# Kernel optimization log

Hardware: AMD Instinct MI355X
Metric: run time of the kernel (lower is better)

The kernel has to match this reference:

```python
import jax, jax.numpy as jnp
import numpy as np

N_WIRES = 4
DIM = 2 ** N_WIRES  # 16-dim statevector


def _zsigns():
    # PauliZ sign per basis state; wire 0 is the most-significant bit
    idx = np.arange(DIM)
    signs = np.stack([1 - 2 * ((idx >> (N_WIRES - 1 - w)) & 1) for w in range(N_WIRES)], 0)
    return jnp.asarray(signs, jnp.float32)  # [4, 16]

ZSIGNS = _zsigns()


def _apply_rx(state, ang, w):
    # state: [B, 16] complex64, ang: [B] rotation angle on wire w
    B = state.shape[0]
    s = state.reshape(B, 2 ** w, 2, 2 ** (N_WIRES - 1 - w))
    c = jnp.cos(ang * 0.5)[:, None, None]
    sn = jnp.sin(ang * 0.5)[:, None, None]
    s0, s1 = s[:, :, 0, :], s[:, :, 1, :]
    o0 = c * s0 - 1j * sn * s1
    o1 = -1j * sn * s0 + c * s1
    return jnp.stack([o0, o1], axis=2).reshape(B, DIM)


def _cnot(state, c, t):
    # flip target bit t where control bit c == 1
    B = state.shape[0]
    s = state.reshape((B,) + (2,) * N_WIRES)
    ca, ta = c + 1, t + 1  # +1 for batch axis
    s0 = jnp.take(s, 0, axis=ca)
    s1 = jnp.take(s, 1, axis=ca)
    t_ax = ta - 1 if ta > ca else ta  # target axis shifts after control axis removed
    s1 = jnp.flip(s1, axis=t_ax)     # size-2 flip == Pauli-X
    return jnp.stack([s0, s1], axis=ca).reshape(B, DIM)


def _qgate(v, theta):
    # v: [B, 4] encoder angles, theta: [4] trainable RX angles (RX angles add)
    B = v.shape[0]
    ang = v + theta[None, :]
    state = jnp.zeros((B, DIM), jnp.complex64).at[:, 0].set(1.0)
    for w in range(N_WIRES):
        state = _apply_rx(state, ang[:, w], w)
    for w in range(N_WIRES):
        state = _cnot(state, w, (w + 1) % N_WIRES)
    probs = jnp.real(state * jnp.conj(state))  # [B, 16]
    return probs @ ZSIGNS.T                    # [B, 4] <Z> per wire


def setup_inputs() -> dict:
    key = jax.random.key(0)
    ks = jax.random.split(key, 16)
    B, S, V, E, H, T = 256, 128, 32000, 256, 4, 32
    d_in = E + H
    sc = 1.0 / np.sqrt(d_in)
    inp = {
        'x': jax.random.randint(ks[0], (B, S), 0, V),
        'embedding': jax.random.normal(ks[1], (V, E), jnp.float32) * 0.02,
        'Wf': jax.random.normal(ks[2], (H, d_in), jnp.float32) * sc,
        'bf': jnp.zeros((H,), jnp.float32),
        'Wi': jax.random.normal(ks[3], (H, d_in), jnp.float32) * sc,
        'bi': jnp.zeros((H,), jnp.float32),
        'Wu': jax.random.normal(ks[4], (H, d_in), jnp.float32) * sc,
        'bu': jnp.zeros((H,), jnp.float32),
        'Wo': jax.random.normal(ks[5], (H, d_in), jnp.float32) * sc,
        'bo': jnp.zeros((H,), jnp.float32),
        'theta_f': jax.random.uniform(ks[6], (H,), jnp.float32, 0.0, 2 * np.pi),
        'theta_i': jax.random.uniform(ks[7], (H,), jnp.float32, 0.0, 2 * np.pi),
        'theta_u': jax.random.uniform(ks[8], (H,), jnp.float32, 0.0, 2 * np.pi),
        'theta_o': jax.random.uniform(ks[9], (H,), jnp.float32, 0.0, 2 * np.pi),
        'Wc': jax.random.normal(ks[10], (T, H), jnp.float32) * 0.5,
        'bc': jnp.zeros((T,), jnp.float32),
    }
    return inp


def reference(x, embedding, Wf, bf, Wi, bi, Wu, bu, Wo, bo,
              theta_f, theta_i, theta_u, theta_o, Wc, bc):
    emb = embedding[x]  # [B, S, E]
    B, S, E = emb.shape
    H = Wf.shape[0]

    def step(carry, xt):
        hx, cx = carry
        comb = jnp.concatenate([xt, hx], axis=1)  # [B, E+H]
        f = jax.nn.sigmoid(_qgate(comb @ Wf.T + bf, theta_f))
        i = jax.nn.sigmoid(_qgate(comb @ Wi.T + bi, theta_i))
        g = jnp.tanh(_qgate(comb @ Wu.T + bu, theta_u))
        o = jax.nn.sigmoid(_qgate(comb @ Wo.T + bo, theta_o))
        cx = f * cx + i * g
        hx = o * jnp.tanh(cx)
        return (hx, cx), hx

    h0 = jnp.zeros((B, H), emb.dtype)
    (_, _), hs = jax.lax.scan(step, (h0, h0), jnp.swapaxes(emb, 0, 1))
    lstm_out = jnp.swapaxes(hs, 0, 1)        # [B, S, H]
    logits = lstm_out @ Wc.T + bc            # [B, S, T]
    return jax.nn.log_softmax(logits, axis=-1)
```

## Files before the change

kernel.cpp:

```cpp
#include <hip/hip_runtime.h>
#include <math.h>

constexpr int NB = 256;
constexpr int NS = 128;
constexpr int NE = 256;
constexpr int DIN = 260;

typedef float f2 __attribute__((ext_vector_type(2)));
#define fma2(A, B, C) __builtin_elementwise_fma((A), (B), (C))

constexpr float INV2PI = 0.15915494309189535f;

__device__ __forceinline__ float rcp_fast(float x) {
#if __has_builtin(__builtin_amdgcn_rcpf)
    return __builtin_amdgcn_rcpf(x);
#else
    return 1.0f / x;
#endif
}

__device__ __forceinline__ float cos_rev(float x) {
    float f, r;
    asm("v_fract_f32 %0, %1" : "=v"(f) : "v"(x));
    asm("v_cos_f32 %0, %1" : "=v"(r) : "v"(f));
    return r;
}

#if __has_builtin(__builtin_amdgcn_mov_dpp)
#define DPP_XOR1(x) __int_as_float(__builtin_amdgcn_mov_dpp(__float_as_int(x), 0xB1, 0xF, 0xF, true))
#define DPP_XOR2(x) __int_as_float(__builtin_amdgcn_mov_dpp(__float_as_int(x), 0x4E, 0xF, 0xF, true))
#define DPP_XOR3(x) __int_as_float(__builtin_amdgcn_mov_dpp(__float_as_int(x), 0x1B, 0xF, 0xF, true))
#else
#define DPP_XOR1(x) __shfl_xor((x), 1, 64)
#define DPP_XOR2(x) __shfl_xor((x), 2, 64)
#define DPP_XOR3(x) __shfl_xor((x), 3, 64)
#endif

__device__ __forceinline__ float tanh_cf(float y) {
    float w = y * y;
    float num = y * fmaf(fmaf(21.0f, w, 1260.0f), w, 10395.0f);
    float den = fmaf(fmaf(w + 210.0f, w, 4725.0f), w, 10395.0f);
    return num * rcp_fast(den);
}

__device__ __forceinline__ float sel4f(float v0, float v1, float v2, float v3,
                                       bool bit0, bool bit1) {
    float lo = bit0 ? v1 : v0;
    float hi = bit0 ? v3 : v2;
    return bit1 ? hi : lo;
}

__global__ __launch_bounds__(256) void k_embed(
    const int* __restrict__ x, const float* __restrict__ emb,
    const float* __restrict__ Wf, const float* __restrict__ bf,
    const float* __restrict__ Wi, const float* __restrict__ bi,
    const float* __restrict__ Wu, const float* __restrict__ bu,
    const float* __restrict__ Wo, const float* __restrict__ bo,
    const float* __restrict__ thf, const float* __restrict__ thi,
    const float* __restrict__ thu, const float* __restrict__ tho,
    float* __restrict__ xpart)
{
    const int lane = threadIdx.x & 63;
    const int wave_id = blockIdx.x * 4 + (threadIdx.x >> 6);
    const int row0 = wave_id * 16;

    const int tok16 = x[((row0 & 255) + (lane & 15)) * NS + (row0 >> 8)];

    float4 Wreg[16];
    #pragma unroll
    for (int j = 0; j < 16; ++j) {
        const float* Wgp = (j < 8) ? ((j < 4) ? Wf : Wi) : ((j < 12) ? Wu : Wo);
        float4 w = *(const float4*)(Wgp + (j & 3) * DIN + lane * 4);
        Wreg[j] = make_float4(w.x * INV2PI, w.y * INV2PI, w.z * INV2PI, w.w * INV2PI);
    }
    float biasv;
    {
        int j = lane & 15, jj = j & 3;
        const float* bp = (j < 8) ? ((j < 4) ? bf : bi) : ((j < 12) ? bu : bo);
        const float* tp = (j < 8) ? ((j < 4) ? thf : thi) : ((j < 12) ? thu : tho);
        biasv = (bp[jj] + tp[jj]) * INV2PI;
    }

    const bool p0 = (lane & 1) != 0, p1 = (lane & 2) != 0,
               p2 = (lane & 4) != 0, p3 = (lane & 8) != 0;

#define LDE(I) (*(const float4*)(emb + \
    (size_t)(unsigned)__shfl(tok16, (I), 64) * NE + lane * 4))

#define PROC(I, EV) do {                                                     \
    float acc[16];                                                           \
    _Pragma("unroll")                                                        \
    for (int j = 0; j < 16; ++j) {                                           \
        float4 wv = Wreg[j];                                                 \
        acc[j] = fmaf((EV).x, wv.x, fmaf((EV).y, wv.y,                       \
                  fmaf((EV).z, wv.z, (EV).w * wv.w)));                       \
    }                                                                        \
    float t8[8];                                                             \
    _Pragma("unroll")                                                        \
    for (int i2 = 0; i2 < 8; ++i2) {                                         \
        float keep = p0 ? acc[2 * i2 + 1] : acc[2 * i2];                     \
        float send = p0 ? acc[2 * i2] : acc[2 * i2 + 1];                     \
        t8[i2] = keep + __shfl_xor(send, 1, 64);                             \
    }                                                                        \
    float t4[4];                                                             \
    _Pragma("unroll")                                                        \
    for (int i2 = 0; i2 < 4; ++i2) {                                         \
        float keep = p1 ? t8[2 * i2 + 1] : t8[2 * i2];                       \
        float send = p1 ? t8[2 * i2] : t8[2 * i2 + 1];                       \
        t4[i2] = keep + __shfl_xor(send, 2, 64);                             \
    }                                                                        \
    float t2[2];                                                             \
    _Pragma("unroll")                                                        \
    for (int i2 = 0; i2 < 2; ++i2) {                                         \
        float keep = p2 ? t4[2 * i2 + 1] : t4[2 * i2];                       \
        float send = p2 ? t4[2 * i2] : t4[2 * i2 + 1];                       \
        t2[i2] = keep + __shfl_xor(send, 4, 64);                             \
    }                                                                        \
    float keep = p3 ? t2[1] : t2[0];                                         \
    float send = p3 ? t2[0] : t2[1];                                         \
    float t1 = keep + __shfl_xor(send, 8, 64);                               \
    t1 += __shfl_xor(t1, 16, 64);                                            \
    t1 += __shfl_xor(t1, 32, 64);                                            \
    if (lane < 16)                                                           \
        xpart[(size_t)(row0 + (I)) * 16 + lane] = t1 + biasv;                \
} while (0)

    float4 ev0 = LDE(0), ev1 = LDE(1), ev2 = LDE(2),
           ev3 = LDE(3), ev4 = LDE(4), ev5 = LDE(5);
    PROC(0,  ev0); ev0 = LDE(6);
    PROC(1,  ev1); ev1 = LDE(7);
    PROC(2,  ev2); ev2 = LDE(8);
    PROC(3,  ev3); ev3 = LDE(9);
    PROC(4,  ev4); ev4 = LDE(10);
    PROC(5,  ev5); ev5 = LDE(11);
    PROC(6,  ev0); ev0 = LDE(12);
    PROC(7,  ev1); ev1 = LDE(13);
    PROC(8,  ev2); ev2 = LDE(14);
    PROC(9,  ev3); ev3 = LDE(15);
    PROC(10, ev4);
    PROC(11, ev5);
    PROC(12, ev0);
    PROC(13, ev1);
    PROC(14, ev2);
    PROC(15, ev3);
#undef PROC
#undef LDE
}

__global__ __launch_bounds__(64) void k_recur(
    const float* __restrict__ Wf, const float* __restrict__ Wi,
    const float* __restrict__ Wu, const float* __restrict__ Wo,
    const float* __restrict__ xpart, float* __restrict__ hs)
{
    __shared__ float hlds[128][64];

    const int lane = threadIdx.x;
    const int g = lane & 3;
    const int b0 = blockIdx.x * 16;

    const float* Wg = (g == 0) ? Wf : ((g == 1) ? Wi : ((g == 2) ? Wu : Wo));
    f2 W01[4], W23[4];
    #pragma unroll
    for (int k = 0; k < 4; ++k) {
        W01[k] = f2{Wg[0 * DIN + 256 + (g ^ k)] * INV2PI,
                    Wg[1 * DIN + 256 + (g ^ k)] * INV2PI};
        W23[k] = f2{Wg[2 * DIN + 256 + (g ^ k)] * INV2PI,
                    Wg[3 * DIN + 256 + (g ^ k)] * INV2PI};
    }

    const bool bb0 = (g & 1) != 0, bb1 = (g & 2) != 0;
    const float scl = (g == 2) ? 1.0f : 0.5f;
    const float mlt = (g == 2) ? 1.0f : 0.5f;
    const float bas = (g == 2) ? 0.0f : 0.5f;
    const float s2 = scl * scl;
    const float e0 = mlt * 0.999416f * scl;
    const float e1 = mlt * -0.326958f * scl * s2;
    const float e2 = mlt * 0.111796f * scl * s2 * s2;
    const float e3 = mlt * -0.022660f * scl * s2 * s2 * s2;
    const f2 D0d = {e0, e0}, D1d = {e1, e1}, D2d = {e2, e2}, D3d = {e3, e3};
    const f2 basd = {bas, bas};

    float c = 0.0f;
    float hr0 = 0.f, hr1 = 0.f, hr2 = 0.f, hr3 = 0.f;

    const char* xblk = (const char*)xpart + (size_t)b0 * 64 + (size_t)lane * 16;

#define LDX(CH, K) (*(const float4*)(xblk + (size_t)(((CH) * 8 + (K)) * 16384)))

#define QS(XC, S) do {                                                        \
    f2 x01 = {(XC).x, (XC).y}, x23 = {(XC).z, (XC).w};                        \
    f2 h0d = {hr0, hr0}, h1d = {hr1, hr1}, h2d = {hr2, hr2}, h3d = {hr3, hr3};\
    f2 a01 = fma2(W01[0], h0d, x01);                                          \
    f2 n01 = W01[2] * h2d;                                                    \
    a01 = fma2(W01[1], h1d, a01);                                             \
    n01 = fma2(W01[3], h3d, n01);                                             \
    a01 = a01 + n01;                                                          \
    f2 a23 = fma2(W23[0], h0d, x23);                                          \
    f2 n23 = W23[2] * h2d;                                                    \
    a23 = fma2(W23[1], h1d, a23);                                             \
    n23 = fma2(W23[3], h3d, n23);                                             \
    a23 = a23 + n23;                                                          \
    float c0_ = cos_rev(a01.x), c1_ = cos_rev(a01.y);                         \
    float c2_ = cos_rev(a23.x), c3_ = cos_rev(a23.y);                         \
    float tt = c2_ * c3_;                                                     \
    float q1 = c0_ * c1_;                                                     \
    f2 q01 = {c1_ * tt, q1};                                                  \
    f2 q23 = {q1 * c2_, q1 * tt};                                             \
    f2 w01 = q01 * q01, w23 = q23 * q23;                                      \
    f2 p01 = fma2(fma2(fma2(D3d, w01, D2d), w01, D1d), w01, D0d);             \
    f2 p23 = fma2(fma2(fma2(D3d, w23, D2d), w23, D1d), w23, D0d);             \
    f2 A01 = fma2(q01, p01, basd);                                            \
    f2 A23 = fma2(q23, p23, basd);                                            \
    float A0 = A01.x, A1 = A01.y, A2 = A23.x, A3 = A23.y;                     \
    float r1 = DPP_XOR1(sel4f(A0, A1, A2, A3, !bb0,  bb1));                   \
    float r2 = DPP_XOR2(sel4f(A0, A1, A2, A3,  bb0, !bb1));                   \
    float r3 = DPP_XOR3(sel4f(A0, A1, A2, A3, !bb0, !bb1));                   \
    float r0 = sel4f(A0, A1, A2, A3, bb0, bb1);                               \
    float fv = sel4f(r0, r1, r2, r3,  bb0,  bb1);                             \
    float iv = sel4f(r0, r1, r2, r3, !bb0,  bb1);                             \
    float uv = sel4f(r0, r1, r2, r3,  bb0, !bb1);                             \
    float ov = sel4f(r0, r1, r2, r3, !bb0, !bb1);                             \
    c = fmaf(fv, c, iv * uv);                                                 \
    float hn = ov * tanh_cf(c);                                               \
    hlds[S][lane] = hn;                                                       \
    hr0 = hn;                                                                 \
    hr1 = DPP_XOR1(hn);                                                       \
    hr2 = DPP_XOR2(hn);                                                       \
    hr3 = DPP_XOR3(hn);                                                       \
} while (0)

    float4 xA0 = LDX(0, 0), xA1 = LDX(0, 1), xA2 = LDX(0, 2), xA3 = LDX(0, 3);
    float4 xA4 = LDX(0, 4), xA5 = LDX(0, 5), xA6 = LDX(0, 6), xA7 = LDX(0, 7);
    float4 xB0 = LDX(1, 0), xB1 = LDX(1, 1), xB2 = LDX(1, 2), xB3 = LDX(1, 3);
    float4 xB4 = LDX(1, 4), xB5 = LDX(1, 5), xB6 = LDX(1, 6), xB7 = LDX(1, 7);

    for (int cp = 0; cp < 7; ++cp) {
        int s0 = cp * 16;
        int chA = cp * 2 + 2;
        int chB = cp * 2 + 3;
        QS(xA0, s0 + 0);  xA0 = LDX(chA, 0);
        QS(xA1, s0 + 1);  xA1 = LDX(chA, 1);
        QS(xA2, s0 + 2);  xA2 = LDX(chA, 2);
        QS(xA3, s0 + 3);  xA3 = LDX(chA, 3);
        QS(xA4, s0 + 4);  xA4 = LDX(chA, 4);
        QS(xA5, s0 + 5);  xA5 = LDX(chA, 5);
        QS(xA6, s0 + 6);  xA6 = LDX(chA, 6);
        QS(xA7, s0 + 7);  xA7 = LDX(chA, 7);
        QS(xB0, s0 + 8);  xB0 = LDX(chB, 0);
        QS(xB1, s0 + 9);  xB1 = LDX(chB, 1);
        QS(xB2, s0 + 10); xB2 = LDX(chB, 2);
        QS(xB3, s0 + 11); xB3 = LDX(chB, 3);
        QS(xB4, s0 + 12); xB4 = LDX(chB, 4);
        QS(xB5, s0 + 13); xB5 = LDX(chB, 5);
        QS(xB6, s0 + 14); xB6 = LDX(chB, 6);
        QS(xB7, s0 + 15); xB7 = LDX(chB, 7);
    }
    QS(xA0, 112); QS(xA1, 113); QS(xA2, 114); QS(xA3, 115);
    QS(xA4, 116); QS(xA5, 117); QS(xA6, 118); QS(xA7, 119);
    QS(xB0, 120); QS(xB1, 121); QS(xB2, 122); QS(xB3, 123);
    QS(xB4, 124); QS(xB5, 125); QS(xB6, 126); QS(xB7, 127);
#undef QS
#undef LDX

    __builtin_amdgcn_s_waitcnt(0);
    #pragma unroll 4
    for (int j = 0; j < 32; ++j) {
        int sp = j * 4 + (lane >> 4);
        float4 v = *(const float4*)&hlds[sp][(lane & 15) * 4];
        *(float4*)(hs + (size_t)sp * 1024 + (size_t)b0 * 4 + (lane & 15) * 4) = v;
    }
}

__global__ __launch_bounds__(256) void k_out(
    const float* __restrict__ hs, const float* __restrict__ Wc,
    const float* __restrict__ bc, float* __restrict__ out)
{
    int gtid = blockIdx.x * 256 + threadIdx.x;
    int r = gtid >> 3;
    int lr = gtid & 7;
    if (r >= NB * NS) return;
    int b = r >> 7, s = r & 127;
    float4 h = *(const float4*)(hs + ((size_t)s * NB + b) * 4);
    float l[4];
    #pragma unroll
    for (int k = 0; k < 4; ++k) {
        int t = lr * 4 + k;
        float4 w = *(const float4*)(Wc + t * 4);
        l[k] = bc[t] + w.x * h.x + w.y * h.y + w.z * h.z + w.w * h.w;
    }
    float m = fmaxf(fmaxf(l[0], l[1]), fmaxf(l[2], l[3]));
    #pragma unroll
    for (int msk = 1; msk < 8; msk <<= 1)
        m = fmaxf(m, __shfl_xor(m, msk, 64));
    float sum = 0.f;
    #pragma unroll
    for (int k = 0; k < 4; ++k)
        sum += __expf(l[k] - m);
    #pragma unroll
    for (int msk = 1; msk < 8; msk <<= 1)
        sum += __shfl_xor(sum, msk, 64);
    float lse = __logf(sum);
    float4 o;
    o.x = l[0] - m - lse;
    o.y = l[1] - m - lse;
    o.z = l[2] - m - lse;
    o.w = l[3] - m - lse;
    *(float4*)(out + (size_t)r * 32 + lr * 4) = o;
}

extern "C" void kernel_launch(void* const* d_in, const int* in_sizes, int n_in,
                              void* d_out, int out_size, void* d_ws, size_t ws_size,
                              hipStream_t stream) {
    const int*   x   = (const int*)d_in[0];
    const float* emb = (const float*)d_in[1];
    const float* Wf  = (const float*)d_in[2];
    const float* bf  = (const float*)d_in[3];
    const float* Wi  = (const float*)d_in[4];
    const float* bi  = (const float*)d_in[5];
    const float* Wu  = (const float*)d_in[6];
    const float* bu  = (const float*)d_in[7];
    const float* Wo  = (const float*)d_in[8];
    const float* bo  = (const float*)d_in[9];
    const float* thf = (const float*)d_in[10];
    const float* thi = (const float*)d_in[11];
    const float* thu = (const float*)d_in[12];
    const float* tho = (const float*)d_in[13];
    const float* Wc  = (const float*)d_in[14];
    const float* bc  = (const float*)d_in[15];
    float* out = (float*)d_out;

    float* xpart = (float*)d_ws;
    float* hs    = xpart + (size_t)NS * NB * 16;

    k_embed<<<512, 256, 0, stream>>>(x, emb, Wf, bf, Wi, bi, Wu, bu, Wo, bo,
                                     thf, thi, thu, tho, xpart);
    k_recur<<<16, 64, 0, stream>>>(Wf, Wi, Wu, Wo, xpart, hs);
    k_out<<<1024, 256, 0, stream>>>(hs, Wc, bc, out);
}
```

Measured before the change: 42.00 us.

## Fuse output projection and log-softmax into recurrence kernel, drop hs buffer

Removes the separate k_out launch and the hs round-trip through global memory. The recurrence block grows to 256 threads: one wave runs the serial LSTM while the others wait at a barrier, then all four waves compute the classifier logits and log-softmax straight from LDS. The embed kernel now loads each token index directly from global memory instead of broadcasting one preloaded index per lane with a shuffle. The trade-off is that only 16 blocks do the output epilogue instead of 1024, and the LDS row is padded to 68 floats to reduce bank conflicts.

```diff
diff --git a/kernel.cpp b/kernel.cpp
--- a/kernel.cpp
+++ b/kernel.cpp
@@ -62,9 +62,6 @@
 {
     const int lane = threadIdx.x & 63;
     const int wave_id = blockIdx.x * 4 + (threadIdx.x >> 6);
-    const int row0 = wave_id * 16;
-
-    const int tok16 = x[((row0 & 255) + (lane & 15)) * NS + (row0 >> 8)];
 
     float4 Wreg[16];
     #pragma unroll
@@ -84,8 +81,10 @@
     const bool p0 = (lane & 1) != 0, p1 = (lane & 2) != 0,
                p2 = (lane & 4) != 0, p3 = (lane & 8) != 0;
 
+    const int row0 = wave_id * 16;
+
 #define LDE(I) (*(const float4*)(emb + \
-    (size_t)(unsigned)__shfl(tok16, (I), 64) * NE + lane * 4))
+    (size_t)x[((row0 + (I)) & 255) * NS + ((row0 + (I)) >> 8)] * NE + lane * 4))
 
 #define PROC(I, EV) do {                                                     \
     float acc[16];                                                           \
@@ -147,43 +146,48 @@
 #undef LDE
 }
 
-__global__ __launch_bounds__(64) void k_recur(
+__global__ __launch_bounds__(256) void k_recur(
     const float* __restrict__ Wf, const float* __restrict__ Wi,
     const float* __restrict__ Wu, const float* __restrict__ Wo,
-    const float* __restrict__ xpart, float* __restrict__ hs)
+    const float* __restrict__ xpart,
+    const float* __restrict__ Wc, const float* __restrict__ bc,
+    float* __restrict__ out)
 {
-    __shared__ float hlds[128][64];
-
-    const int lane = threadIdx.x;
-    const int g = lane & 3;
+    __shared__ float hlds[128][68];
+
+    const int tid = threadIdx.x;
+    const int lane = tid & 63;
     const int b0 = blockIdx.x * 16;
 
-    const float* Wg = (g == 0) ? Wf : ((g == 1) ? Wi : ((g == 2) ? Wu : Wo));
-    f2 W01[4], W23[4];
-    #pragma unroll
-    for (int k = 0; k < 4; ++k) {
-        W01[k] = f2{Wg[0 * DIN + 256 + (g ^ k)] * INV2PI,
-                    Wg[1 * DIN + 256 + (g ^ k)] * INV2PI};
-        W23[k] = f2{Wg[2 * DIN + 256 + (g ^ k)] * INV2PI,
-                    Wg[3 * DIN + 256 + (g ^ k)] * INV2PI};
-    }
-
-    const bool bb0 = (g & 1) != 0, bb1 = (g & 2) != 0;
-    const float scl = (g == 2) ? 1.0f : 0.5f;
-    const float mlt = (g == 2) ? 1.0f : 0.5f;
-    const float bas = (g == 2) ? 0.0f : 0.5f;
-    const float s2 = scl * scl;
-    const float e0 = mlt * 0.999416f * scl;
-    const float e1 = mlt * -0.326958f * scl * s2;
-    const float e2 = mlt * 0.111796f * scl * s2 * s2;
-    const float e3 = mlt * -0.022660f * scl * s2 * s2 * s2;
-    const f2 D0d = {e0, e0}, D1d = {e1, e1}, D2d = {e2, e2}, D3d = {e3, e3};
-    const f2 basd = {bas, bas};
-
-    float c = 0.0f;
-    float hr0 = 0.f, hr1 = 0.f, hr2 = 0.f, hr3 = 0.f;
-
-    const char* xblk = (const char*)xpart + (size_t)b0 * 64 + (size_t)lane * 16;
+    if (tid < 64) {
+        const int g = lane & 3;
+
+        const float* Wg = (g == 0) ? Wf : ((g == 1) ? Wi : ((g == 2) ? Wu : Wo));
+        f2 W01[4], W23[4];
+        #pragma unroll
+        for (int k = 0; k < 4; ++k) {
+            W01[k] = f2{Wg[0 * DIN + 256 + (g ^ k)] * INV2PI,
+                        Wg[1 * DIN + 256 + (g ^ k)] * INV2PI};
+            W23[k] = f2{Wg[2 * DIN + 256 + (g ^ k)] * INV2PI,
+                        Wg[3 * DIN + 256 + (g ^ k)] * INV2PI};
+        }
+
+        const bool bb0 = (g & 1) != 0, bb1 = (g & 2) != 0;
+        const float scl = (g == 2) ? 1.0f : 0.5f;
+        const float mlt = (g == 2) ? 1.0f : 0.5f;
+        const float bas = (g == 2) ? 0.0f : 0.5f;
+        const float s2 = scl * scl;
+        const float e0 = mlt * 0.999416f * scl;
+        const float e1 = mlt * -0.326958f * scl * s2;
+        const float e2 = mlt * 0.111796f * scl * s2 * s2;
+        const float e3 = mlt * -0.022660f * scl * s2 * s2 * s2;
+        const f2 D0d = {e0, e0}, D1d = {e1, e1}, D2d = {e2, e2}, D3d = {e3, e3};
+        const f2 basd = {bas, bas};
+
+        float c = 0.0f;
+        float hr0 = 0.f, hr1 = 0.f, hr2 = 0.f, hr3 = 0.f;
+
+        const char* xblk = (const char*)xpart + (size_t)b0 * 64 + (size_t)lane * 16;
 
 #define LDX(CH, K) (*(const float4*)(xblk + (size_t)(((CH) * 8 + (K)) * 16384)))
 
@@ -229,83 +233,71 @@
     hr3 = DPP_XOR3(hn);                                                       \
 } while (0)
 
-    float4 xA0 = LDX(0, 0), xA1 = LDX(0, 1), xA2 = LDX(0, 2), xA3 = LDX(0, 3);
-    float4 xA4 = LDX(0, 4), xA5 = LDX(0, 5), xA6 = LDX(0, 6), xA7 = LDX(0, 7);
-    float4 xB0 = LDX(1, 0), xB1 = LDX(1, 1), xB2 = LDX(1, 2), xB3 = LDX(1, 3);
-    float4 xB4 = LDX(1, 4), xB5 = LDX(1, 5), xB6 = LDX(1, 6), xB7 = LDX(1, 7);
-
-    for (int cp = 0; cp < 7; ++cp) {
-        int s0 = cp * 16;
-        int chA = cp * 2 + 2;
-        int chB = cp * 2 + 3;
-        QS(xA0, s0 + 0);  xA0 = LDX(chA, 0);
-        QS(xA1, s0 + 1);  xA1 = LDX(chA, 1);
-        QS(xA2, s0 + 2);  xA2 = LDX(chA, 2);
-        QS(xA3, s0 + 3);  xA3 = LDX(chA, 3);
-        QS(xA4, s0 + 4);  xA4 = LDX(chA, 4);
-        QS(xA5, s0 + 5);  xA5 = LDX(chA, 5);
-        QS(xA6, s0 + 6);  xA6 = LDX(chA, 6);
-        QS(xA7, s0 + 7);  xA7 = LDX(chA, 7);
-        QS(xB0, s0 + 8);  xB0 = LDX(chB, 0);
-        QS(xB1, s0 + 9);  xB1 = LDX(chB, 1);
-        QS(xB2, s0 + 10); xB2 = LDX(chB, 2);
-        QS(xB3, s0 + 11); xB3 = LDX(chB, 3);
-        QS(xB4, s0 + 12); xB4 = LDX(chB, 4);
-        QS(xB5, s0 + 13); xB5 = LDX(chB, 5);
-        QS(xB6, s0 + 14); xB6 = LDX(chB, 6);
-        QS(xB7, s0 + 15); xB7 = LDX(chB, 7);
-    }
-    QS(xA0, 112); QS(xA1, 113); QS(xA2, 114); QS(xA3, 115);
-    QS(xA4, 116); QS(xA5, 117); QS(xA6, 118); QS(xA7, 119);
-    QS(xB0, 120); QS(xB1, 121); QS(xB2, 122); QS(xB3, 123);
-    QS(xB4, 124); QS(xB5, 125); QS(xB6, 126); QS(xB7, 127);
+        float4 xA0 = LDX(0, 0), xA1 = LDX(0, 1), xA2 = LDX(0, 2), xA3 = LDX(0, 3);
+        float4 xA4 = LDX(0, 4), xA5 = LDX(0, 5), xA6 = LDX(0, 6), xA7 = LDX(0, 7);
+        float4 xB0 = LDX(1, 0), xB1 = LDX(1, 1), xB2 = LDX(1, 2), xB3 = LDX(1, 3);
+        float4 xB4 = LDX(1, 4), xB5 = LDX(1, 5), xB6 = LDX(1, 6), xB7 = LDX(1, 7);
+
+        for (int cp = 0; cp < 7; ++cp) {
+            int s0 = cp * 16;
+            int chA = cp * 2 + 2;
+            int chB = cp * 2 + 3;
+            QS(xA0, s0 + 0);  xA0 = LDX(chA, 0);
+            QS(xA1, s0 + 1);  xA1 = LDX(chA, 1);
+            QS(xA2, s0 + 2);  xA2 = LDX(chA, 2);
+            QS(xA3, s0 + 3);  xA3 = LDX(chA, 3);
+            QS(xA4, s0 + 4);  xA4 = LDX(chA, 4);
+            QS(xA5, s0 + 5);  xA5 = LDX(chA, 5);
+            QS(xA6, s0 + 6);  xA6 = LDX(chA, 6);
+            QS(xA7, s0 + 7);  xA7 = LDX(chA, 7);
+            QS(xB0, s0 + 8);  xB0 = LDX(chB, 0);
+            QS(xB1, s0 + 9);  xB1 = LDX(chB, 1);
+            QS(xB2, s0 + 10); xB2 = LDX(chB, 2);
+            QS(xB3, s0 + 11); xB3 = LDX(chB, 3);
+            QS(xB4, s0 + 12); xB4 = LDX(chB, 4);
+            QS(xB5, s0 + 13); xB5 = LDX(chB, 5);
+            QS(xB6, s0 + 14); xB6 = LDX(chB, 6);
+            QS(xB7, s0 + 15); xB7 = LDX(chB, 7);
+        }
+        QS(xA0, 112); QS(xA1, 113); QS(xA2, 114); QS(xA3, 115);
+        QS(xA4, 116); QS(xA5, 117); QS(xA6, 118); QS(xA7, 119);
+        QS(xB0, 120); QS(xB1, 121); QS(xB2, 122); QS(xB3, 123);
+        QS(xB4, 124); QS(xB5, 125); QS(xB6, 126); QS(xB7, 127);
 #undef QS
 #undef LDX
-
-    __builtin_amdgcn_s_waitcnt(0);
+    }
+
+    __syncthreads();
+
+    const int t0 = (tid & 7) * 4;
+    float4 w0 = *(const float4*)(Wc + (t0 + 0) * 4);
+    float4 w1 = *(const float4*)(Wc + (t0 + 1) * 4);
+    float4 w2 = *(const float4*)(Wc + (t0 + 2) * 4);
+    float4 w3 = *(const float4*)(Wc + (t0 + 3) * 4);
+    float4 bv = *(const float4*)(bc + t0);
+
     #pragma unroll 4
-    for (int j = 0; j < 32; ++j) {
-        int sp = j * 4 + (lane >> 4);
-        float4 v = *(const float4*)&hlds[sp][(lane & 15) * 4];
-        *(float4*)(hs + (size_t)sp * 1024 + (size_t)b0 * 4 + (lane & 15) * 4) = v;
+    for (int pass = 0; pass < 64; ++pass) {
+        int r = pass * 32 + (tid >> 3);
+        int bat = r >> 7, s = r & 127;
+        float4 h4 = *(const float4*)&hlds[s][bat * 4];
+        float l0 = bv.x + w0.x * h4.x + w0.y * h4.y + w0.z * h4.z + w0.w * h4.w;
+        float l1 = bv.y + w1.x * h4.x + w1.y * h4.y + w1.z * h4.z + w1.w * h4.w;
+        float l2 = bv.z + w2.x * h4.x + w2.y * h4.y + w2.z * h4.z + w2.w * h4.w;
+        float l3 = bv.w + w3.x * h4.x + w3.y * h4.y + w3.z * h4.z + w3.w * h4.w;
+        float m = fmaxf(fmaxf(l0, l1), fmaxf(l2, l3));
+        m = fmaxf(m, __shfl_xor(m, 1, 64));
+        m = fmaxf(m, __shfl_xor(m, 2, 64));
+        m = fmaxf(m, __shfl_xor(m, 4, 64));
+        float sum = __expf(l0 - m) + __expf(l1 - m) + __expf(l2 - m) + __expf(l3 - m);
+        sum += __shfl_xor(sum, 1, 64);
+        sum += __shfl_xor(sum, 2, 64);
+        sum += __shfl_xor(sum, 4, 64);
+        float base = m + __logf(sum);
+        float4 o;
+        o.x = l0 - base; o.y = l1 - base; o.z = l2 - base; o.w = l3 - base;
+        *(float4*)(out + ((size_t)(b0 + bat) * 128 + s) * 32 + t0) = o;
     }
-}
-
-__global__ __launch_bounds__(256) void k_out(
-    const float* __restrict__ hs, const float* __restrict__ Wc,
-    const float* __restrict__ bc, float* __restrict__ out)
-{
-    int gtid = blockIdx.x * 256 + threadIdx.x;
-    int r = gtid >> 3;
-    int lr = gtid & 7;
-    if (r >= NB * NS) return;
-    int b = r >> 7, s = r & 127;
-    float4 h = *(const float4*)(hs + ((size_t)s * NB + b) * 4);
-    float l[4];
-    #pragma unroll
-    for (int k = 0; k < 4; ++k) {
-        int t = lr * 4 + k;
-        float4 w = *(const float4*)(Wc + t * 4);
-        l[k] = bc[t] + w.x * h.x + w.y * h.y + w.z * h.z + w.w * h.w;
-    }
-    float m = fmaxf(fmaxf(l[0], l[1]), fmaxf(l[2], l[3]));
-    #pragma unroll
-    for (int msk = 1; msk < 8; msk <<= 1)
-        m = fmaxf(m, __shfl_xor(m, msk, 64));
-    float sum = 0.f;
-    #pragma unroll
-    for (int k = 0; k < 4; ++k)
-        sum += __expf(l[k] - m);
-    #pragma unroll
-    for (int msk = 1; msk < 8; msk <<= 1)
-        sum += __shfl_xor(sum, msk, 64);
-    float lse = __logf(sum);
-    float4 o;
-    o.x = l[0] - m - lse;
-    o.y = l[1] - m - lse;
-    o.z = l[2] - m - lse;
-    o.w = l[3] - m - lse;
-    *(float4*)(out + (size_t)r * 32 + lr * 4) = o;
 }
 
 extern "C" void kernel_launch(void* const* d_in, const int* in_sizes, int n_in,
@@ -330,10 +322,8 @@
     float* out = (float*)d_out;
 
     float* xpart = (float*)d_ws;
-    float* hs    = xpart + (size_t)NS * NB * 16;
 
     k_embed<<<512, 256, 0, stream>>>(x, emb, Wf, bf, Wi, bi, Wu, bu, Wo, bo,
                                      thf, thi, thu, tho, xpart);
-    k_recur<<<16, 64, 0, stream>>>(Wf, Wi, Wu, Wo, xpart, hs);
-    k_out<<<1024, 256, 0, stream>>>(hs, Wc, bc, out);
-}
+    k_recur<<<16, 256, 0, stream>>>(Wf, Wi, Wu, Wo, xpart, Wc, bc, out);
+}
```

Measured after the change: 50.70 us. +20.7%, slower.

## Fuse embedding projection and recurrence with per-chunk atomic counters

Applied to the files above, without the earlier changes.

Merges the embedding-projection kernel and the recurrent kernel into one launch. Sixteen blocks run the recurrence and spin on atomic counters until each chunk of projected inputs is ready, while the remaining blocks compute projections and signal completion with release atomics. The aim is to overlap the serial recurrence with the parallel projection work and remove a kernel boundary. The cost is an extra memset, smaller 64-thread producer blocks, and reliance on the recurrence blocks being co-resident with the producers, which risks spin overhead or deadlock if they are not.

```diff
diff --git a/kernel.cpp b/kernel.cpp
--- a/kernel.cpp
+++ b/kernel.cpp
@@ -50,7 +50,7 @@
     return bit1 ? hi : lo;
 }
 
-__global__ __launch_bounds__(256) void k_embed(
+__global__ __launch_bounds__(64) void k_fused(
     const int* __restrict__ x, const float* __restrict__ emb,
     const float* __restrict__ Wf, const float* __restrict__ bf,
     const float* __restrict__ Wi, const float* __restrict__ bi,
@@ -58,34 +58,33 @@
     const float* __restrict__ Wo, const float* __restrict__ bo,
     const float* __restrict__ thf, const float* __restrict__ thi,
     const float* __restrict__ thu, const float* __restrict__ tho,
-    float* __restrict__ xpart)
+    float* xpart, float* __restrict__ hs, int* cnt)
 {
-    const int lane = threadIdx.x & 63;
-    const int wave_id = blockIdx.x * 4 + (threadIdx.x >> 6);
-    const int row0 = wave_id * 16;
-
-    const int tok16 = x[((row0 & 255) + (lane & 15)) * NS + (row0 >> 8)];
-
-    float4 Wreg[16];
-    #pragma unroll
-    for (int j = 0; j < 16; ++j) {
-        const float* Wgp = (j < 8) ? ((j < 4) ? Wf : Wi) : ((j < 12) ? Wu : Wo);
-        float4 w = *(const float4*)(Wgp + (j & 3) * DIN + lane * 4);
-        Wreg[j] = make_float4(w.x * INV2PI, w.y * INV2PI, w.z * INV2PI, w.w * INV2PI);
-    }
-    float biasv;
-    {
-        int j = lane & 15, jj = j & 3;
-        const float* bp = (j < 8) ? ((j < 4) ? bf : bi) : ((j < 12) ? bu : bo);
-        const float* tp = (j < 8) ? ((j < 4) ? thf : thi) : ((j < 12) ? thu : tho);
-        biasv = (bp[jj] + tp[jj]) * INV2PI;
-    }
-
-    const bool p0 = (lane & 1) != 0, p1 = (lane & 2) != 0,
-               p2 = (lane & 4) != 0, p3 = (lane & 8) != 0;
+    const int lane = threadIdx.x;
+
+    if (blockIdx.x >= 16) {
+        const int u = blockIdx.x - 16;
+        const int row0 = u * 16;
+
+        float4 Wreg[16];
+        #pragma unroll
+        for (int j = 0; j < 16; ++j) {
+            const float* Wgp = (j < 8) ? ((j < 4) ? Wf : Wi) : ((j < 12) ? Wu : Wo);
+            float4 w = *(const float4*)(Wgp + (j & 3) * DIN + lane * 4);
+            Wreg[j] = make_float4(w.x * INV2PI, w.y * INV2PI, w.z * INV2PI, w.w * INV2PI);
+        }
+        float biasv;
+        {
+            int j = lane & 15, jj = j & 3;
+            const float* bp = (j < 8) ? ((j < 4) ? bf : bi) : ((j < 12) ? bu : bo);
+            const float* tp = (j < 8) ? ((j < 4) ? thf : thi) : ((j < 12) ? thu : tho);
+            biasv = (bp[jj] + tp[jj]) * INV2PI;
+        }
+        const bool p0 = (lane & 1) != 0, p1 = (lane & 2) != 0,
+                   p2 = (lane & 4) != 0, p3 = (lane & 8) != 0;
 
 #define LDE(I) (*(const float4*)(emb + \
-    (size_t)(unsigned)__shfl(tok16, (I), 64) * NE + lane * 4))
+    (size_t)x[((row0 + (I)) & 255) * NS + ((row0 + (I)) >> 8)] * NE + lane * 4))
 
 #define PROC(I, EV) do {                                                     \
     float acc[16];                                                           \
@@ -125,38 +124,47 @@
         xpart[(size_t)(row0 + (I)) * 16 + lane] = t1 + biasv;                \
 } while (0)
 
-    float4 ev0 = LDE(0), ev1 = LDE(1), ev2 = LDE(2),
-           ev3 = LDE(3), ev4 = LDE(4), ev5 = LDE(5);
-    PROC(0,  ev0); ev0 = LDE(6);
-    PROC(1,  ev1); ev1 = LDE(7);
-    PROC(2,  ev2); ev2 = LDE(8);
-    PROC(3,  ev3); ev3 = LDE(9);
-    PROC(4,  ev4); ev4 = LDE(10);
-    PROC(5,  ev5); ev5 = LDE(11);
-    PROC(6,  ev0); ev0 = LDE(12);
-    PROC(7,  ev1); ev1 = LDE(13);
-    PROC(8,  ev2); ev2 = LDE(14);
-    PROC(9,  ev3); ev3 = LDE(15);
-    PROC(10, ev4);
-    PROC(11, ev5);
-    PROC(12, ev0);
-    PROC(13, ev1);
-    PROC(14, ev2);
-    PROC(15, ev3);
+        float4 ev0 = LDE(0), ev1 = LDE(1), ev2 = LDE(2),
+               ev3 = LDE(3), ev4 = LDE(4), ev5 = LDE(5);
+        PROC(0,  ev0); ev0 = LDE(6);
+        PROC(1,  ev1); ev1 = LDE(7);
+        PROC(2,  ev2); ev2 = LDE(8);
+        PROC(3,  ev3); ev3 = LDE(9);
+        PROC(4,  ev4); ev4 = LDE(10);
+        PROC(5,  ev5); ev5 = LDE(11);
+        PROC(6,  ev0); ev0 = LDE(12);
+        PROC(7,  ev1); ev1 = LDE(13);
+        PROC(8,  ev2); ev2 = LDE(14);
+        PROC(9,  ev3); ev3 = LDE(15);
+        PROC(10, ev4);
+        PROC(11, ev5);
+        PROC(12, ev0);
+        PROC(13, ev1);
+        PROC(14, ev2);
+        PROC(15, ev3);
 #undef PROC
 #undef LDE
-}
-
-__global__ __launch_bounds__(64) void k_recur(
-    const float* __restrict__ Wf, const float* __restrict__ Wi,
-    const float* __restrict__ Wu, const float* __restrict__ Wo,
-    const float* __restrict__ xpart, float* __restrict__ hs)
-{
+
+        __threadfence();
+        if (lane == 0)
+            __hip_atomic_fetch_add(&cnt[u >> 4], 1, __ATOMIC_RELEASE,
+                                   __HIP_MEMORY_SCOPE_AGENT);
+        return;
+    }
+
     __shared__ float hlds[128][64];
 
-    const int lane = threadIdx.x;
     const int g = lane & 3;
     const int b0 = blockIdx.x * 16;
+
+    auto wait_chunk = [&](int CH) {
+        const int idx = CH * 8 + (lane & 7);
+        for (;;) {
+            int v = __hip_atomic_load(&cnt[idx], __ATOMIC_ACQUIRE,
+                                      __HIP_MEMORY_SCOPE_AGENT);
+            if (__all(v == 16)) break;
+        }
+    };
 
     const float* Wg = (g == 0) ? Wf : ((g == 1) ? Wi : ((g == 2) ? Wu : Wo));
     f2 W01[4], W23[4];
@@ -229,6 +237,8 @@
     hr3 = DPP_XOR3(hn);                                                       \
 } while (0)
 
+    wait_chunk(0);
+    wait_chunk(1);
     float4 xA0 = LDX(0, 0), xA1 = LDX(0, 1), xA2 = LDX(0, 2), xA3 = LDX(0, 3);
     float4 xA4 = LDX(0, 4), xA5 = LDX(0, 5), xA6 = LDX(0, 6), xA7 = LDX(0, 7);
     float4 xB0 = LDX(1, 0), xB1 = LDX(1, 1), xB2 = LDX(1, 2), xB3 = LDX(1, 3);
@@ -238,6 +248,8 @@
         int s0 = cp * 16;
         int chA = cp * 2 + 2;
         int chB = cp * 2 + 3;
+        wait_chunk(chA);
+        wait_chunk(chB);
         QS(xA0, s0 + 0);  xA0 = LDX(chA, 0);
         QS(xA1, s0 + 1);  xA1 = LDX(chA, 1);
         QS(xA2, s0 + 2);  xA2 = LDX(chA, 2);
@@ -331,9 +343,10 @@
 
     float* xpart = (float*)d_ws;
     float* hs    = xpart + (size_t)NS * NB * 16;
-
-    k_embed<<<512, 256, 0, stream>>>(x, emb, Wf, bf, Wi, bi, Wu, bu, Wo, bo,
-                                     thf, thi, thu, tho, xpart);
-    k_recur<<<16, 64, 0, stream>>>(Wf, Wi, Wu, Wo, xpart, hs);
+    int*   cnt   = (int*)(hs + (size_t)NS * NB * 4);
+
+    hipMemsetAsync(cnt, 0, 128 * sizeof(int), stream);
+    k_fused<<<2064, 64, 0, stream>>>(x, emb, Wf, bf, Wi, bi, Wu, bu, Wo, bo,
+                                     thf, thi, thu, tho, xpart, hs, cnt);
     k_out<<<1024, 256, 0, stream>>>(hs, Wc, bc, out);
 }
```

New measurement: 103.2 us. 2.46x slower.
